# Performance work log

Hardware: AMD Instinct MI355X
Metric: run time of the kernel (lower is better)

Reference implementation:

```python
import jax, jax.numpy as jnp
import numpy as np

NUM_EXPERTS = 64
TOP_K = 6
ALPHA = 1e-3
HIDDEN = 128


def setup_inputs() -> dict:
    key = jax.random.key(0)
    k1, k2 = jax.random.split(key)
    hidden_states = jax.random.normal(k1, (64, 4096, HIDDEN), dtype=jnp.float32)
    # kaiming_uniform_(a=sqrt(5)) on weight of shape (64, 128): bound = 1/sqrt(fan_in)
    bound = 1.0 / np.sqrt(HIDDEN)
    W = jax.random.uniform(k2, (NUM_EXPERTS, HIDDEN), dtype=jnp.float32, minval=-bound, maxval=bound)
    return {"hidden_states": hidden_states, "W": W}


def reference(hidden_states, W):
    b, s, h = hidden_states.shape
    x = hidden_states.reshape(-1, h)                      # (N, h)
    logits = x @ W.T                                      # (N, 64)
    scores = jax.nn.softmax(logits, axis=-1)
    topk_weight, topk_idx = jax.lax.top_k(scores, TOP_K)  # (N, 6)
    # norm_topk_prob=True
    topk_weight = topk_weight / (topk_weight.sum(-1, keepdims=True) + 1e-20)
    # aux loss (training path, seq_aux=False): ce = one_hot(topk_idx).mean(0)
    counts = jnp.zeros(NUM_EXPERTS, dtype=scores.dtype).at[topk_idx.ravel()].add(1.0)
    ce = counts / jnp.asarray(topk_idx.size, scores.dtype)
    Pi = scores.mean(0)
    fi = ce * NUM_EXPERTS
    aux_loss = (Pi * fi).sum() * ALPHA
    return topk_idx, topk_weight, aux_loss
```

## Files before the change

kernel.cpp:

```cpp
#include <hip/hip_runtime.h>
#include <cfloat>

#define NTOK (64 * 4096)
#define HID  128
#define NE   64
#define TK   6
#define BLK  256
#define TPB  256
#define GRID (NTOK / TPB)
#define LST  67

__global__ __launch_bounds__(BLK, 2)
void gate_kernel(const float* __restrict__ X,
                 const float* __restrict__ W,
                 float* __restrict__ oidx,
                 float* __restrict__ ow,
                 float* __restrict__ Pi_g,
                 unsigned int* __restrict__ cnt_g)
{
    __shared__ float        smem[TPB * LST];
    __shared__ float        mz[2 * TPB];
    __shared__ float        Pi_s[NE];
    __shared__ unsigned int cnt_s[NE];

    const int tid  = threadIdx.x;
    const int lane = tid & 63;
    const int wv   = __builtin_amdgcn_readfirstlane(tid >> 6);
    const int eb   = wv * 16;

    if (tid < NE) cnt_s[tid] = 0u;

    {
        const float4* W4 = (const float4*)W;
#pragma unroll
        for (int i = 0; i < 8; ++i) {
            const int flat = tid + i * BLK;
            const float4 v = W4[flat];
            const int e   = flat >> 5;
            const int c   = flat & 31;
            const int col = (e + ((c & 15) << 2)) & 63;
            float* p = &smem[c * 256 + col];
            p[0]   = v.x;
            p[64]  = v.y;
            p[128] = v.z;
            p[192] = v.w;
        }
    }
    __syncthreads();

    const int gtok0 = blockIdx.x * TPB;
    const float4* xr0 = (const float4*)(X + (size_t)(gtok0 + lane      ) * HID);
    const float4* xr1 = (const float4*)(X + (size_t)(gtok0 + lane +  64) * HID);
    const float4* xr2 = (const float4*)(X + (size_t)(gtok0 + lane + 128) * HID);
    const float4* xr3 = (const float4*)(X + (size_t)(gtok0 + lane + 192) * HID);

    float acc[4][16];
#pragma unroll
    for (int g = 0; g < 4; ++g)
#pragma unroll
        for (int j = 0; j < 16; ++j) acc[g][j] = 0.0f;

#pragma unroll 2
    for (int c = 0; c < 32; ++c) {
        float xs[4][4];
        {
            const float4 v0 = xr0[c], v1 = xr1[c], v2 = xr2[c], v3 = xr3[c];
            xs[0][0]=v0.x; xs[0][1]=v0.y; xs[0][2]=v0.z; xs[0][3]=v0.w;
            xs[1][0]=v1.x; xs[1][1]=v1.y; xs[1][2]=v1.z; xs[1][3]=v1.w;
            xs[2][0]=v2.x; xs[2][1]=v2.y; xs[2][2]=v2.z; xs[2][3]=v2.w;
            xs[3][0]=v3.x; xs[3][1]=v3.y; xs[3][2]=v3.z; xs[3][3]=v3.w;
        }
        const int rr = (c & 15) << 2;
        const int c0 = (eb +  0 + rr) & 63;
        const int c1 = (eb +  4 + rr) & 63;
        const int c2 = (eb +  8 + rr) & 63;
        const int c3 = (eb + 12 + rr) & 63;
        const float* rowb = &smem[c * 256];
#pragma unroll
        for (int d = 0; d < 4; ++d) {
            const float* row = rowb + d * 64;
            const float4 w0 = *(const float4*)&row[c0];
            const float4 w1 = *(const float4*)&row[c1];
            const float4 w2 = *(const float4*)&row[c2];
            const float4 w3 = *(const float4*)&row[c3];
#pragma unroll
            for (int g = 0; g < 4; ++g) {
                const float xv = xs[g][d];
                acc[g][ 0] = fmaf(xv, w0.x, acc[g][ 0]);
                acc[g][ 1] = fmaf(xv, w0.y, acc[g][ 1]);
                acc[g][ 2] = fmaf(xv, w0.z, acc[g][ 2]);
                acc[g][ 3] = fmaf(xv, w0.w, acc[g][ 3]);
                acc[g][ 4] = fmaf(xv, w1.x, acc[g][ 4]);
                acc[g][ 5] = fmaf(xv, w1.y, acc[g][ 5]);
                acc[g][ 6] = fmaf(xv, w1.z, acc[g][ 6]);
                acc[g][ 7] = fmaf(xv, w1.w, acc[g][ 7]);
                acc[g][ 8] = fmaf(xv, w2.x, acc[g][ 8]);
                acc[g][ 9] = fmaf(xv, w2.y, acc[g][ 9]);
                acc[g][10] = fmaf(xv, w2.z, acc[g][10]);
                acc[g][11] = fmaf(xv, w2.w, acc[g][11]);
                acc[g][12] = fmaf(xv, w3.x, acc[g][12]);
                acc[g][13] = fmaf(xv, w3.y, acc[g][13]);
                acc[g][14] = fmaf(xv, w3.z, acc[g][14]);
                acc[g][15] = fmaf(xv, w3.w, acc[g][15]);
            }
        }
    }

    __syncthreads();

#pragma unroll
    for (int g = 0; g < 4; ++g) {
        float* p = &smem[(lane + 64 * g) * LST + eb];
#pragma unroll
        for (int j = 0; j < 16; ++j) p[j] = acc[g][j];
    }
    __syncthreads();

    {
        const int t = tid;
        const float* Lrow = &smem[t * LST];
        float tv[TK]; int ti[TK];
#pragma unroll
        for (int q = 0; q < TK; ++q) { tv[q] = -FLT_MAX; ti[q] = 0; }

#pragma unroll 8
        for (int e = 0; e < NE; ++e) {
            float m = Lrow[e];
            int   mi = e;
#pragma unroll
            for (int q = 0; q < TK; ++q) {
                const bool  cx = m > tv[q];
                const float nt = cx ? m     : tv[q];
                const float nm = cx ? tv[q] : m;
                const int   ni = cx ? mi    : ti[q];
                const int   nj = cx ? ti[q] : mi;
                tv[q] = nt; m = nm; ti[q] = ni; mi = nj;
            }
        }

        const float mx = tv[0];
        float ex[TK]; float s = 0.0f;
#pragma unroll
        for (int q = 0; q < TK; ++q) { ex[q] = __expf(tv[q] - mx); s += ex[q]; }
        const float rs = 1.0f / (s + 1e-20f);

        const size_t gt = (size_t)(gtok0 + t) * TK;
        float2* ip = (float2*)(oidx + gt);
        float2* wp = (float2*)(ow + gt);
        ip[0] = make_float2((float)ti[0], (float)ti[1]);
        ip[1] = make_float2((float)ti[2], (float)ti[3]);
        ip[2] = make_float2((float)ti[4], (float)ti[5]);
        wp[0] = make_float2(ex[0]*rs, ex[1]*rs);
        wp[1] = make_float2(ex[2]*rs, ex[3]*rs);
        wp[2] = make_float2(ex[4]*rs, ex[5]*rs);

#pragma unroll
        for (int q = 0; q < TK; ++q) atomicAdd(&cnt_s[ti[q]], 1u);

        float Z = 0.0f;
#pragma unroll 8
        for (int e = 0; e < NE; ++e) Z += __expf(Lrow[e] - mx);
        mz[2*t]     = mx;
        mz[2*t + 1] = 1.0f / Z;
    }
    __syncthreads();

    {
        float pi[16];
#pragma unroll
        for (int j = 0; j < 16; ++j) pi[j] = 0.0f;
#pragma unroll
        for (int g = 0; g < 4; ++g) {
            const int t = lane + 64 * g;
            const float mxt = mz[2*t];
            const float rzt = mz[2*t + 1];
            const float* p = &smem[t * LST + eb];
#pragma unroll
            for (int j = 0; j < 16; ++j)
                pi[j] += __expf(p[j] - mxt) * rzt;
        }
#pragma unroll
        for (int s = 1; s <= 32; s <<= 1) {
#pragma unroll
            for (int j = 0; j < 16; ++j) pi[j] += __shfl_xor(pi[j], s);
        }
        if (lane < 16) Pi_s[eb + lane] = pi[lane];
    }
    __syncthreads();

    if (tid < NE) {
        atomicAdd(&Pi_g[tid], Pi_s[tid]);
        atomicAdd(&cnt_g[tid], cnt_s[tid]);
    }
}

__global__ void aux_kernel(const float* __restrict__ Pi_g,
                           const unsigned int* __restrict__ cnt_g,
                           float* __restrict__ out_aux)
{
    const int e = threadIdx.x;
    const float Pi = Pi_g[e] * (1.0f / (float)NTOK);
    const float ce = (float)cnt_g[e] * (1.0f / (float)(NTOK * TK));
    float v = Pi * ce * (float)NE;
#pragma unroll
    for (int off = 32; off > 0; off >>= 1) v += __shfl_down(v, off);
    if (e == 0) out_aux[0] = v * 1.0e-3f;
}

extern "C" void kernel_launch(void* const* d_in, const int* in_sizes, int n_in,
                              void* d_out, int out_size, void* d_ws, size_t ws_size,
                              hipStream_t stream) {
    const float* X = (const float*)d_in[0];
    const float* W = (const float*)d_in[1];

    float* out  = (float*)d_out;
    float* oidx = out;
    float* ow   = out + (size_t)NTOK * TK;
    float* aux  = out + (size_t)NTOK * TK * 2;

    float*        Pi_g  = (float*)d_ws;
    unsigned int* cnt_g = (unsigned int*)((char*)d_ws + 256);

    hipMemsetAsync(d_ws, 0, 512, stream);
    gate_kernel<<<GRID, BLK, 0, stream>>>(X, W, oidx, ow, Pi_g, cnt_g);
    aux_kernel<<<1, 64, 0, stream>>>(Pi_g, cnt_g, aux);
}
```

Baseline: 257.8 us.

## Halve logits LDS staging via two-pass online softmax and prefetch X/W

Stages the 256x64 logits tile through shared memory in two 32-expert halves, cutting LDS from about 67KB to 33KB. Each half computes a partial top-k and a partial softmax sum, and the two sums are merged online. Launch bounds rise from 2 to 3 blocks per CU, and the Pi pass reads logits from registers instead of LDS. The X row and W float4 loads are software-prefetched with the loop unroll set to 1; this costs extra barriers and more register pressure under the tighter launch bound.

```diff
diff --git a/kernel.cpp b/kernel.cpp
--- a/kernel.cpp
+++ b/kernel.cpp
@@ -8,9 +8,9 @@
 #define BLK  256
 #define TPB  256
 #define GRID (NTOK / TPB)
-#define LST  67
-
-__global__ __launch_bounds__(BLK, 2)
+#define TST  33
+
+__global__ __launch_bounds__(BLK, 3)
 void gate_kernel(const float* __restrict__ X,
                  const float* __restrict__ W,
                  float* __restrict__ oidx,
@@ -18,7 +18,7 @@
                  float* __restrict__ Pi_g,
                  unsigned int* __restrict__ cnt_g)
 {
-    __shared__ float        smem[TPB * LST];
+    __shared__ float        smem[TPB * TST];
     __shared__ float        mz[2 * TPB];
     __shared__ float        Pi_s[NE];
     __shared__ unsigned int cnt_s[NE];
@@ -60,71 +60,84 @@
 #pragma unroll
         for (int j = 0; j < 16; ++j) acc[g][j] = 0.0f;
 
-#pragma unroll 2
+    float4 nx0 = xr0[0], nx1 = xr1[0], nx2 = xr2[0], nx3 = xr3[0];
+
+#pragma unroll 1
     for (int c = 0; c < 32; ++c) {
         float xs[4][4];
-        {
-            const float4 v0 = xr0[c], v1 = xr1[c], v2 = xr2[c], v3 = xr3[c];
-            xs[0][0]=v0.x; xs[0][1]=v0.y; xs[0][2]=v0.z; xs[0][3]=v0.w;
-            xs[1][0]=v1.x; xs[1][1]=v1.y; xs[1][2]=v1.z; xs[1][3]=v1.w;
-            xs[2][0]=v2.x; xs[2][1]=v2.y; xs[2][2]=v2.z; xs[2][3]=v2.w;
-            xs[3][0]=v3.x; xs[3][1]=v3.y; xs[3][2]=v3.z; xs[3][3]=v3.w;
-        }
+        xs[0][0]=nx0.x; xs[0][1]=nx0.y; xs[0][2]=nx0.z; xs[0][3]=nx0.w;
+        xs[1][0]=nx1.x; xs[1][1]=nx1.y; xs[1][2]=nx1.z; xs[1][3]=nx1.w;
+        xs[2][0]=nx2.x; xs[2][1]=nx2.y; xs[2][2]=nx2.z; xs[2][3]=nx2.w;
+        xs[3][0]=nx3.x; xs[3][1]=nx3.y; xs[3][2]=nx3.z; xs[3][3]=nx3.w;
+
+        const int cn = (c < 31) ? (c + 1) : 0;
+        nx0 = xr0[cn]; nx1 = xr1[cn]; nx2 = xr2[cn]; nx3 = xr3[cn];
+
         const int rr = (c & 15) << 2;
-        const int c0 = (eb +  0 + rr) & 63;
-        const int c1 = (eb +  4 + rr) & 63;
-        const int c2 = (eb +  8 + rr) & 63;
-        const int c3 = (eb + 12 + rr) & 63;
         const float* rowb = &smem[c * 256];
+        const float* p0 = &rowb[(eb +  0 + rr) & 63];
+        const float* p1 = &rowb[(eb +  4 + rr) & 63];
+        const float* p2 = &rowb[(eb +  8 + rr) & 63];
+        const float* p3 = &rowb[(eb + 12 + rr) & 63];
+
+        float4 wA0 = *(const float4*)(p0);
+        float4 wA1 = *(const float4*)(p1);
+        float4 wA2 = *(const float4*)(p2);
+        float4 wA3 = *(const float4*)(p3);
+
 #pragma unroll
         for (int d = 0; d < 4; ++d) {
-            const float* row = rowb + d * 64;
-            const float4 w0 = *(const float4*)&row[c0];
-            const float4 w1 = *(const float4*)&row[c1];
-            const float4 w2 = *(const float4*)&row[c2];
-            const float4 w3 = *(const float4*)&row[c3];
+            float4 wB0, wB1, wB2, wB3;
+            if (d < 3) {
+                wB0 = *(const float4*)(p0 + 64*(d+1));
+                wB1 = *(const float4*)(p1 + 64*(d+1));
+                wB2 = *(const float4*)(p2 + 64*(d+1));
+                wB3 = *(const float4*)(p3 + 64*(d+1));
+            }
 #pragma unroll
             for (int g = 0; g < 4; ++g) {
                 const float xv = xs[g][d];
-                acc[g][ 0] = fmaf(xv, w0.x, acc[g][ 0]);
-                acc[g][ 1] = fmaf(xv, w0.y, acc[g][ 1]);
-                acc[g][ 2] = fmaf(xv, w0.z, acc[g][ 2]);
-                acc[g][ 3] = fmaf(xv, w0.w, acc[g][ 3]);
-                acc[g][ 4] = fmaf(xv, w1.x, acc[g][ 4]);
-                acc[g][ 5] = fmaf(xv, w1.y, acc[g][ 5]);
-                acc[g][ 6] = fmaf(xv, w1.z, acc[g][ 6]);
-                acc[g][ 7] = fmaf(xv, w1.w, acc[g][ 7]);
-                acc[g][ 8] = fmaf(xv, w2.x, acc[g][ 8]);
-                acc[g][ 9] = fmaf(xv, w2.y, acc[g][ 9]);
-                acc[g][10] = fmaf(xv, w2.z, acc[g][10]);
-                acc[g][11] = fmaf(xv, w2.w, acc[g][11]);
-                acc[g][12] = fmaf(xv, w3.x, acc[g][12]);
-                acc[g][13] = fmaf(xv, w3.y, acc[g][13]);
-                acc[g][14] = fmaf(xv, w3.z, acc[g][14]);
-                acc[g][15] = fmaf(xv, w3.w, acc[g][15]);
-            }
-        }
-    }
-
-    __syncthreads();
-
-#pragma unroll
-    for (int g = 0; g < 4; ++g) {
-        float* p = &smem[(lane + 64 * g) * LST + eb];
-#pragma unroll
-        for (int j = 0; j < 16; ++j) p[j] = acc[g][j];
-    }
-    __syncthreads();
-
-    {
-        const int t = tid;
-        const float* Lrow = &smem[t * LST];
-        float tv[TK]; int ti[TK];
-#pragma unroll
-        for (int q = 0; q < TK; ++q) { tv[q] = -FLT_MAX; ti[q] = 0; }
-
-#pragma unroll 8
-        for (int e = 0; e < NE; ++e) {
+                acc[g][ 0] = fmaf(xv, wA0.x, acc[g][ 0]);
+                acc[g][ 1] = fmaf(xv, wA0.y, acc[g][ 1]);
+                acc[g][ 2] = fmaf(xv, wA0.z, acc[g][ 2]);
+                acc[g][ 3] = fmaf(xv, wA0.w, acc[g][ 3]);
+                acc[g][ 4] = fmaf(xv, wA1.x, acc[g][ 4]);
+                acc[g][ 5] = fmaf(xv, wA1.y, acc[g][ 5]);
+                acc[g][ 6] = fmaf(xv, wA1.z, acc[g][ 6]);
+                acc[g][ 7] = fmaf(xv, wA1.w, acc[g][ 7]);
+                acc[g][ 8] = fmaf(xv, wA2.x, acc[g][ 8]);
+                acc[g][ 9] = fmaf(xv, wA2.y, acc[g][ 9]);
+                acc[g][10] = fmaf(xv, wA2.z, acc[g][10]);
+                acc[g][11] = fmaf(xv, wA2.w, acc[g][11]);
+                acc[g][12] = fmaf(xv, wA3.x, acc[g][12]);
+                acc[g][13] = fmaf(xv, wA3.y, acc[g][13]);
+                acc[g][14] = fmaf(xv, wA3.z, acc[g][14]);
+                acc[g][15] = fmaf(xv, wA3.w, acc[g][15]);
+            }
+            if (d < 3) { wA0 = wB0; wA1 = wB1; wA2 = wB2; wA3 = wB3; }
+        }
+    }
+
+    __syncthreads();
+
+    float tv[TK]; int ti[TK];
+#pragma unroll
+    for (int q = 0; q < TK; ++q) { tv[q] = -FLT_MAX; ti[q] = 0; }
+    float m0, s0, m1, s1;
+
+    if (wv < 2) {
+#pragma unroll
+        for (int g = 0; g < 4; ++g) {
+            float* p = &smem[(lane + 64*g) * TST + eb];
+#pragma unroll
+            for (int j = 0; j < 16; ++j) p[j] = acc[g][j];
+        }
+    }
+    __syncthreads();
+    {
+        const float* Lrow = &smem[tid * TST];
+#pragma unroll 8
+        for (int e = 0; e < 32; ++e) {
             float m = Lrow[e];
             int   mi = e;
 #pragma unroll
@@ -137,14 +150,59 @@
                 tv[q] = nt; m = nm; ti[q] = ni; mi = nj;
             }
         }
-
+        m0 = tv[0];
+        float ss = 0.0f;
+#pragma unroll 8
+        for (int e = 0; e < 32; ++e) ss += __expf(Lrow[e] - m0);
+        s0 = ss;
+    }
+    __syncthreads();
+
+    if (wv >= 2) {
+#pragma unroll
+        for (int g = 0; g < 4; ++g) {
+            float* p = &smem[(lane + 64*g) * TST + (eb - 32)];
+#pragma unroll
+            for (int j = 0; j < 16; ++j) p[j] = acc[g][j];
+        }
+    }
+    __syncthreads();
+    {
+        const float* Lrow = &smem[tid * TST];
+        float pm = -FLT_MAX;
+#pragma unroll 8
+        for (int e2 = 0; e2 < 32; ++e2) {
+            float m = Lrow[e2];
+            pm = fmaxf(pm, m);
+            int mi = 32 + e2;
+#pragma unroll
+            for (int q = 0; q < TK; ++q) {
+                const bool  cx = m > tv[q];
+                const float nt = cx ? m     : tv[q];
+                const float nm = cx ? tv[q] : m;
+                const int   ni = cx ? mi    : ti[q];
+                const int   nj = cx ? ti[q] : mi;
+                tv[q] = nt; m = nm; ti[q] = ni; mi = nj;
+            }
+        }
+        m1 = pm;
+        float ss = 0.0f;
+#pragma unroll 8
+        for (int e2 = 0; e2 < 32; ++e2) ss += __expf(Lrow[e2] - m1);
+        s1 = ss;
+    }
+
+    {
         const float mx = tv[0];
+        const float Z  = s0 * __expf(m0 - mx) + s1 * __expf(m1 - mx);
+        const float rz = 1.0f / Z;
+
         float ex[TK]; float s = 0.0f;
 #pragma unroll
         for (int q = 0; q < TK; ++q) { ex[q] = __expf(tv[q] - mx); s += ex[q]; }
         const float rs = 1.0f / (s + 1e-20f);
 
-        const size_t gt = (size_t)(gtok0 + t) * TK;
+        const size_t gt = (size_t)(gtok0 + tid) * TK;
         float2* ip = (float2*)(oidx + gt);
         float2* wp = (float2*)(ow + gt);
         ip[0] = make_float2((float)ti[0], (float)ti[1]);
@@ -157,11 +215,8 @@
 #pragma unroll
         for (int q = 0; q < TK; ++q) atomicAdd(&cnt_s[ti[q]], 1u);
 
-        float Z = 0.0f;
-#pragma unroll 8
-        for (int e = 0; e < NE; ++e) Z += __expf(Lrow[e] - mx);
-        mz[2*t]     = mx;
-        mz[2*t + 1] = 1.0f / Z;
+        mz[2*tid]     = mx;
+        mz[2*tid + 1] = rz;
     }
     __syncthreads();
 
@@ -174,10 +229,9 @@
             const int t = lane + 64 * g;
             const float mxt = mz[2*t];
             const float rzt = mz[2*t + 1];
-            const float* p = &smem[t * LST + eb];
 #pragma unroll
             for (int j = 0; j < 16; ++j)
-                pi[j] += __expf(p[j] - mxt) * rzt;
+                pi[j] += __expf(acc[g][j] - mxt) * rzt;
         }
 #pragma unroll
         for (int s = 1; s <= 32; s <<= 1) {
```

Measured after the change: 285.4 us. 1.11x slower.
